# Performance work log

Measured on AMD Instinct MI355X. Metric: run time of the kernel, lower is better.

## Reference

```python
import jax, jax.numpy as jnp
import numpy as np

MAX_SEQ = 2048   # text_max_length: pre-allocated cache length
B = 16           # beam*batch
H = 32           # head_num
D = 128          # head_dim
OFFSET = 2047    # tokens already stored in the cache (decode at last step)
SCALE = float(np.sqrt(D))  # scale_attn = sqrt(head_size), per docstring


def setup_inputs() -> dict:
    key = jax.random.key(0)
    ks = jax.random.split(key, 6)
    query = jax.random.normal(ks[0], (B, 1, H, D), dtype=jnp.float32)
    key_t = jax.random.normal(ks[1], (B, 1, H, D), dtype=jnp.float32)
    value = jax.random.normal(ks[2], (B, 1, H, D), dtype=jnp.float32)
    key_cache = jax.random.normal(ks[3], (MAX_SEQ, B, H, D), dtype=jnp.float32)
    value_cache = jax.random.normal(ks[4], (MAX_SEQ, B, H, D), dtype=jnp.float32)
    # beam_idx[t, b] = parent beam (cache row) of beam b chosen at step t
    beam_idx = jax.random.randint(ks[5], (MAX_SEQ, B), 0, B, dtype=jnp.int32)
    # additive attention mask over [past + current] positions (zeros = no masking;
    # single-token decode query attends to everything causally anyway)
    attention_mask = jnp.zeros((B, 1, 1, OFFSET + 1), dtype=jnp.float32)
    return {
        "query": query, "key": key_t, "value": value,
        "key_cache": key_cache, "value_cache": value_cache,
        "beam_idx": beam_idx, "attention_mask": attention_mask,
        "offset": OFFSET,
    }


def _beam_trace(beam_idx, offset):
    # Back-trace beam ancestry from the latest step to step 0.
    # trace[t, b] = row in the pre-allocated cache that holds token t of the
    # sequence currently occupying beam slot b.
    def step(cur, bi_t):
        new = bi_t[cur]
        return new, new
    init = jnp.arange(B, dtype=beam_idx.dtype)
    _, trace = jax.lax.scan(step, init, beam_idx[:offset], reverse=True)
    return trace  # [offset, B]


def reference(query, key, value, key_cache, value_cache, beam_idx, attention_mask, offset):
    # Indirect gather of KV history via beam-idx indirection.
    trace = _beam_trace(beam_idx, offset)                      # [offset, B]
    idx = trace[:, :, None, None]                              # broadcast over H, D
    k_hist = jnp.take_along_axis(key_cache[:offset], idx, axis=1)   # [offset, B, H, D]
    v_hist = jnp.take_along_axis(value_cache[:offset], idx, axis=1)
    # Append the current token's key/value (equivalent to writing it into the
    # cache at position `offset` and reading it back).
    k_full = jnp.concatenate([k_hist, jnp.transpose(key, (1, 0, 2, 3))], axis=0)    # [offset+1, B, H, D]
    v_full = jnp.concatenate([v_hist, jnp.transpose(value, (1, 0, 2, 3))], axis=0)
    # Scaled dot-product attention (q_len = 1).
    scores = jnp.einsum('bqhd,tbhd->bhqt', query, k_full) / SCALE  # [B, H, 1, offset+1]
    scores = scores + attention_mask
    probs = jax.nn.softmax(scores, axis=-1)
    attn_output = jnp.einsum('bhqt,tbhd->bqhd', probs, v_full)     # [B, 1, H, D]
    return attn_output
```

## Files before the change

kernel.cpp:

```cpp
#include <hip/hip_runtime.h>
#include <math.h>

#define BEAMS 16
#define TMAX  2048
#define HH    32
#define DD    128
#define NSP   24
#define TSM   88
#define KLD   136
#define WLD   40

typedef float          f32x4 __attribute__((ext_vector_type(4)));
typedef short          s16x8 __attribute__((ext_vector_type(8)));
typedef unsigned short u16x8 __attribute__((ext_vector_type(8)));

__device__ __forceinline__ unsigned short f2bf(float f) {
    unsigned x = __float_as_uint(f);
    return (unsigned short)((x + 0x7FFFu + ((x >> 16) & 1u)) >> 16);
}

__device__ __forceinline__ int kofs(int g, int j) {
    return (j < 4) ? (g * 4 + j) : (16 + g * 4 + (j - 4));
}

__global__ __launch_bounds__(1024)
void trace_kernel(const int* __restrict__ beam_idx,
                  const int* __restrict__ offp,
                  int* __restrict__ trace_tb,
                  unsigned long long* __restrict__ slot4_g,
                  int* __restrict__ rowstart_g,
                  int* __restrict__ rows_tu,
                  int* __restrict__ ucnt_g) {
    const int off = *offp;
    const int T   = off + 1;
    const int C   = 8;
    const int NC  = (off + C - 1) / C;

    __shared__ int S[2][256][BEAMS];
    __shared__ unsigned short seen_s[TMAX];

    const int tid = threadIdx.x;
    const int g   = tid >> 4;
    const int j   = tid & 15;
    const int c0 = g, c1 = g + 64, c2 = g + 128, c3 = g + 192;

    {
        int cur0 = j, cur1 = j, cur2 = j, cur3 = j;
        const int hi0 = (c0 < NC) ? min((c0 + 1) * C, off) : 0;
        const int hi1 = (c1 < NC) ? min((c1 + 1) * C, off) : 0;
        const int hi2 = (c2 < NC) ? min((c2 + 1) * C, off) : 0;
        const int hi3 = (c3 < NC) ? min((c3 + 1) * C, off) : 0;
        const int lo0 = c0 * C, lo1 = c1 * C, lo2 = c2 * C, lo3 = c3 * C;
        for (int i = 0; i < C; ++i) {
            const int ta = hi0 - 1 - i;
            if (c0 < NC && ta >= lo0) cur0 = beam_idx[ta * BEAMS + cur0];
            const int tb = hi1 - 1 - i;
            if (c1 < NC && tb >= lo1) cur1 = beam_idx[tb * BEAMS + cur1];
            const int tc = hi2 - 1 - i;
            if (c2 < NC && tc >= lo2) cur2 = beam_idx[tc * BEAMS + cur2];
            const int td = hi3 - 1 - i;
            if (c3 < NC && td >= lo3) cur3 = beam_idx[td * BEAMS + cur3];
        }
        if (c0 < NC) S[0][c0][j] = cur0;
        if (c1 < NC) S[0][c1][j] = cur1;
        if (c2 < NC) S[0][c2][j] = cur2;
        if (c3 < NC) S[0][c3][j] = cur3;
    }
    __syncthreads();

    int rb = 0;
    for (int step = 1; step < NC; step <<= 1) {
        const int wb = rb ^ 1;
        for (int c = g; c < NC; c += 64) {
            int v;
            if (c + step < NC) v = S[rb][c][ S[rb][c + step][j] ];
            else               v = S[rb][c][j];
            S[wb][c][j] = v;
        }
        __syncthreads();
        rb = wb;
    }

    {
        int cur0 = (c0 + 1 < NC) ? S[rb][c0 + 1][j] : j;
        int cur1 = (c1 + 1 < NC) ? S[rb][c1 + 1][j] : j;
        int cur2 = (c2 + 1 < NC) ? S[rb][c2 + 1][j] : j;
        int cur3 = (c3 + 1 < NC) ? S[rb][c3 + 1][j] : j;
        const int hi0 = (c0 < NC) ? min((c0 + 1) * C, off) : 0;
        const int hi1 = (c1 < NC) ? min((c1 + 1) * C, off) : 0;
        const int hi2 = (c2 < NC) ? min((c2 + 1) * C, off) : 0;
        const int hi3 = (c3 < NC) ? min((c3 + 1) * C, off) : 0;
        const int lo0 = c0 * C, lo1 = c1 * C, lo2 = c2 * C, lo3 = c3 * C;
        for (int i = 0; i < C; ++i) {
            const int ta = hi0 - 1 - i;
            if (c0 < NC && ta >= lo0) {
                cur0 = beam_idx[ta * BEAMS + cur0];
                trace_tb[ta * BEAMS + j] = cur0;
            }
            const int tb = hi1 - 1 - i;
            if (c1 < NC && tb >= lo1) {
                cur1 = beam_idx[tb * BEAMS + cur1];
                trace_tb[tb * BEAMS + j] = cur1;
            }
            const int tc = hi2 - 1 - i;
            if (c2 < NC && tc >= lo2) {
                cur2 = beam_idx[tc * BEAMS + cur2];
                trace_tb[tc * BEAMS + j] = cur2;
            }
            const int td = hi3 - 1 - i;
            if (c3 < NC && td >= lo3) {
                cur3 = beam_idx[td * BEAMS + cur3];
                trace_tb[td * BEAMS + j] = cur3;
            }
        }
    }
    __syncthreads();

    for (int t = tid; t < T; t += 1024) {
        if (t == off) {
            seen_s[t]  = 0xFFFFu;
            slot4_g[t] = 0xFEDCBA9876543210ull;
        } else {
            unsigned seen = 0;
            int us[16];
            #pragma unroll
            for (int b2 = 0; b2 < 16; ++b2) {
                us[b2] = trace_tb[t * BEAMS + b2];
                seen |= 1u << us[b2];
            }
            unsigned long long s4 = 0;
            #pragma unroll
            for (int b2 = 0; b2 < 16; ++b2) {
                const unsigned long long sl =
                    (unsigned long long)__popc(seen & ((1u << us[b2]) - 1u));
                s4 |= sl << (4 * b2);
            }
            seen_s[t]  = (unsigned short)seen;
            slot4_g[t] = s4;
        }
    }
    __syncthreads();

    {
        const int wid  = tid >> 6;
        const int lane = tid & 63;
        const int TS   = (T + NSP - 1) / NSP;
        for (int s = wid; s < NSP; s += 16) {
            const int ts0 = s * TS;
            const int ts1 = min(ts0 + TS, T);
            int cum = 0;
            for (int tc0 = ts0; tc0 < ts1; tc0 += 64) {
                const int t = tc0 + lane;
                const bool valid = (t < ts1);
                const unsigned seen = valid ? (unsigned)seen_s[t] : 0u;
                int x = __popc(seen);
                const int n = x;
                #pragma unroll
                for (int o = 1; o < 64; o <<= 1) {
                    const int y = __shfl_up(x, o, 64);
                    if (lane >= o) x += y;
                }
                const int base = cum + x - n;
                if (valid) {
                    rowstart_g[t] = base;
                    int k = 0;
                    for (unsigned m = seen; m; m &= m - 1) {
                        rows_tu[s * 2048 + base + k] = t * 32 + (__ffs(m) - 1);
                        ++k;
                    }
                }
                cum += __shfl(x, 63, 64);
            }
            if (lane == 0) ucnt_g[s] = cum;
        }
    }
}

__device__ __forceinline__ void pv_step(int pb, int w, int n16, int g4,
                                        const unsigned short (&Wt)[2][16][WLD],
                                        const unsigned short (&Vb)[2][32][KLD],
                                        f32x4 (&accO)[4]) {
    union { unsigned long long qw[2]; s16x8 v; } uw;
    uw.qw[0] = *(const unsigned long long*)(&Wt[pb][n16][g4 * 4]);
    uw.qw[1] = *(const unsigned long long*)(&Wt[pb][n16][16 + g4 * 4]);
    #pragma unroll
    for (int dt = 0; dt < 4; ++dt) {
        const int d = ((w - 2) * 4 + dt) * 16 + n16;
        s16x8 bf;
        #pragma unroll
        for (int jj = 0; jj < 8; ++jj)
            bf[jj] = (short)Vb[pb][kofs(g4, jj)][d];
        accO[dt] = __builtin_amdgcn_mfma_f32_16x16x32_bf16(uw.v, bf, accO[dt], 0, 0, 0);
    }
}

__global__ __launch_bounds__(256, 3)
void attn_split_kernel(const float* __restrict__ q,
                       const float* __restrict__ knew,
                       const float* __restrict__ vnew,
                       const float* __restrict__ kc,
                       const float* __restrict__ vc,
                       const float* __restrict__ mask,
                       const unsigned long long* __restrict__ slot4_g,
                       const int* __restrict__ rowstart_g,
                       const int* __restrict__ rows_tu,
                       const int* __restrict__ ucnt_g,
                       const int* __restrict__ offp,
                       float* __restrict__ pl,
                       float* __restrict__ po) {
    const int off = *offp;
    const int T   = off + 1;
    const int TS  = (T + NSP - 1) / NSP;
    const int h   = blockIdx.x / NSP;
    const int s   = blockIdx.x - h * NSP;
    const int ts0 = s * TS;
    const int ts1 = min(ts0 + TS, T);
    const int nts = ts1 - ts0;
    const int U   = ucnt_g[s];
    const int G   = (U + 31) >> 5;

    __shared__ unsigned short Kb[2][32][KLD];
    __shared__ unsigned short Vb[2][32][KLD];
    __shared__ unsigned short Wt[2][16][WLD];
    __shared__ float mask_s[16][TSM];
    __shared__ unsigned long long slot4_s[TSM];
    __shared__ int   rbase_s[TSM];
    __shared__ float ls[2][16];

    const int tid = threadIdx.x;
    const int w   = tid >> 6;
    const int l   = tid & 63;
    const int n16 = l & 15;
    const int g4  = l >> 4;

    for (int i = tid; i < 16 * TSM; i += 256) {
        const int bb = i / TSM, tt = i - bb * TSM;
        mask_s[bb][tt] = (tt < nts) ? mask[(size_t)bb * T + ts0 + tt] : 0.f;
    }
    for (int i = tid; i < nts; i += 256) {
        slot4_s[i] = slot4_g[ts0 + i];
        rbase_s[i] = rowstart_g[ts0 + i];
    }

    const float inv_scale = 0.08838834764831843f;
    s16x8 qf[4];
    {
        const float* qp = q + ((size_t)(n16 * HH + h)) * DD;
        #pragma unroll
        for (int c = 0; c < 4; ++c) {
            const int base = 32 * c + g4 * 4;
            const float4 lo = *(const float4*)(qp + base);
            const float4 hi = *(const float4*)(qp + base + 16);
            qf[c][0] = (short)f2bf(lo.x * inv_scale);
            qf[c][1] = (short)f2bf(lo.y * inv_scale);
            qf[c][2] = (short)f2bf(lo.z * inv_scale);
            qf[c][3] = (short)f2bf(lo.w * inv_scale);
            qf[c][4] = (short)f2bf(hi.x * inv_scale);
            qf[c][5] = (short)f2bf(hi.y * inv_scale);
            qf[c][6] = (short)f2bf(hi.z * inv_scale);
            qf[c][7] = (short)f2bf(hi.w * inv_scale);
        }
    }

    const int r1 = tid >> 4;
    const int cc = tid & 15;
    float4 sk1a, sk1b, sv1a, sv1b, sk2a, sk2b, sv2a, sv2b;

#define LOADR(UU, KA, KB, VA, VB)                                            \
    {                                                                        \
        const int uu = (UU);                                                 \
        const int tu = (uu < U) ? rows_tu[s * 2048 + uu] : 0;                \
        const int t_ = tu >> 5, u_ = tu & 31;                                \
        const float *ks, *vs;                                                \
        if (t_ < off) {                                                      \
            const size_t ro = ((size_t)(t_ * BEAMS + u_) * HH + h) * DD;     \
            ks = kc + ro; vs = vc + ro;                                      \
        } else {                                                             \
            const size_t ro = ((size_t)u_ * HH + h) * DD;                    \
            ks = knew + ro; vs = vnew + ro;                                  \
        }                                                                    \
        KA = *(const float4*)(ks + cc * 8);                                  \
        KB = *(const float4*)(ks + cc * 8 + 4);                              \
        VA = *(const float4*)(vs + cc * 8);                                  \
        VB = *(const float4*)(vs + cc * 8 + 4);                              \
    }

#define PACK8(DST, A, B)                                                     \
    {                                                                        \
        u16x8 p_;                                                            \
        p_[0] = f2bf(A.x); p_[1] = f2bf(A.y); p_[2] = f2bf(A.z);             \
        p_[3] = f2bf(A.w); p_[4] = f2bf(B.x); p_[5] = f2bf(B.y);             \
        p_[6] = f2bf(B.z); p_[7] = f2bf(B.w);                                \
        *(u16x8*)(DST) = p_;                                                 \
    }

    f32x4 accO[4];
    #pragma unroll
    for (int dt = 0; dt < 4; ++dt) accO[dt] = (f32x4){0.f, 0.f, 0.f, 0.f};
    float l_acc = 0.f;

    __syncthreads();

    if (G > 0) { LOADR(0 * 32 + r1, sk1a, sk1b, sv1a, sv1b)
                 LOADR(0 * 32 + r1 + 16, sk2a, sk2b, sv2a, sv2b) }

    for (int g = 0; g < G; ++g) {
        const int buf = g & 1;
        PACK8(&Kb[buf][r1][cc * 8],      sk1a, sk1b)
        PACK8(&Vb[buf][r1][cc * 8],      sv1a, sv1b)
        PACK8(&Kb[buf][r1 + 16][cc * 8], sk2a, sk2b)
        PACK8(&Vb[buf][r1 + 16][cc * 8], sv2a, sv2b)
        if (g + 1 < G) {
            LOADR((g + 1) * 32 + r1, sk1a, sk1b, sv1a, sv1b)
            LOADR((g + 1) * 32 + r1 + 16, sk2a, sk2b, sv2a, sv2b)
        }
        __syncthreads();

        if (w < 2) {
            f32x4 acc = {0.f, 0.f, 0.f, 0.f};
            const unsigned short* krow = &Kb[buf][w * 16 + n16][0];
            #pragma unroll
            for (int c = 0; c < 4; ++c) {
                const unsigned short* ka = krow + 32 * c + g4 * 4;
                union { unsigned long long qw[2]; s16x8 v; } ua;
                ua.qw[0] = *(const unsigned long long*)(ka);
                ua.qw[1] = *(const unsigned long long*)(ka + 16);
                acc = __builtin_amdgcn_mfma_f32_16x16x32_bf16(ua.v, qf[c], acc, 0, 0, 0);
            }
            unsigned short wout[4];
            #pragma unroll
            for (int r = 0; r < 4; ++r) {
                const int u_loc = g * 32 + w * 16 + g4 * 4 + r;
                const bool valid = (u_loc < U);
                const int tu = valid ? rows_tu[s * 2048 + u_loc] : 0;
                const int t_ = tu >> 5;
                int tt = t_ - ts0;
                tt = (tt < 0) ? 0 : tt;
                const unsigned long long s4 = slot4_s[tt];
                const int myslot = (int)((s4 >> (4 * n16)) & 15);
                const int expsl  = u_loc - rbase_s[tt];
                const bool match = valid && (myslot == expsl);
                const float sc = acc[r] + mask_s[n16][tt];
                const float wv = match ? __expf(sc) : 0.f;
                l_acc += wv;
                wout[r] = f2bf(wv);
            }
            const int wc = w * 16 + g4 * 4;
            *(unsigned*)&Wt[buf][n16][wc]     = (unsigned)wout[0] | ((unsigned)wout[1] << 16);
            *(unsigned*)&Wt[buf][n16][wc + 2] = (unsigned)wout[2] | ((unsigned)wout[3] << 16);
        } else if (g > 0) {
            pv_step(buf ^ 1, w, n16, g4, Wt, Vb, accO);
        }
        __syncthreads();
    }
    if (G > 0 && w >= 2) {
        pv_step((G - 1) & 1, w, n16, g4, Wt, Vb, accO);
    }
#undef LOADR
#undef PACK8

    if (w < 2) {
        l_acc += __shfl_xor(l_acc, 16, 64);
        l_acc += __shfl_xor(l_acc, 32, 64);
        if (l < 16) ls[w][n16] = l_acc;
    }
    __syncthreads();
    if (tid < 16)
        pl[((size_t)tid * HH + h) * NSP + s] = ls[0][tid] + ls[1][tid];

    if (w >= 2) {
        #pragma unroll
        for (int dt = 0; dt < 4; ++dt) {
            const int d = ((w - 2) * 4 + dt) * 16 + n16;
            #pragma unroll
            for (int r = 0; r < 4; ++r) {
                const int b = g4 * 4 + r;
                po[((size_t)(b * HH + h) * NSP + s) * DD + d] = accO[dt][r];
            }
        }
    }
}

__global__ __launch_bounds__(128)
void attn_reduce_kernel(const float* __restrict__ pl,
                        const float* __restrict__ po,
                        float* __restrict__ out) {
    const int bh = blockIdx.x;
    const int d  = threadIdx.x;
    float l = 0.f, o = 0.f;
    #pragma unroll 8
    for (int s = 0; s < NSP; ++s) {
        l += pl[(size_t)bh * NSP + s];
        o += po[((size_t)bh * NSP + s) * DD + d];
    }
    out[(size_t)bh * DD + d] = o / l;
}

extern "C" void kernel_launch(void* const* d_in, const int* in_sizes, int n_in,
                              void* d_out, int out_size, void* d_ws, size_t ws_size,
                              hipStream_t stream) {
    const float* q    = (const float*)d_in[0];
    const float* knew = (const float*)d_in[1];
    const float* vnew = (const float*)d_in[2];
    const float* kc   = (const float*)d_in[3];
    const float* vc   = (const float*)d_in[4];
    const int*   bidx = (const int*)d_in[5];
    const float* mask = (const float*)d_in[6];
    const int*   offp = (const int*)d_in[7];

    char* ws = (char*)d_ws;
    int*                trace_tb = (int*)(ws);
    unsigned long long* slot4    = (unsigned long long*)(ws + 131072);
    int*                rowstart = (int*)(ws + 147456);
    int*                rows_tu  = (int*)(ws + 155648);
    int*                ucnt_g   = (int*)(ws + 352256);
    float*              pl       = (float*)(ws + 352768);
    float*              po       = (float*)(ws + 401920);

    hipLaunchKernelGGL(trace_kernel, dim3(1), dim3(1024), 0, stream,
                       bidx, offp, trace_tb, slot4, rowstart, rows_tu,
                       ucnt_g);
    hipLaunchKernelGGL(attn_split_kernel, dim3(HH * NSP), dim3(256), 0, stream,
                       q, knew, vnew, kc, vc, mask,
                       slot4, rowstart, rows_tu, ucnt_g, offp,
                       pl, po);
    hipLaunchKernelGGL(attn_reduce_kernel, dim3(BEAMS * HH), dim3(128), 0, stream,
                       pl, po, (float*)d_out);
}
```

Baseline: 53.54 us.

## Balance split-K partitions by unique cache-row count instead of equal token spans

```diff
diff --git a/kernel.cpp b/kernel.cpp
--- a/kernel.cpp
+++ b/kernel.cpp
@@ -6,7 +6,7 @@
 #define HH    32
 #define DD    128
 #define NSP   24
-#define TSM   88
+#define TSM   128
 #define KLD   136
 #define WLD   40
 
@@ -30,6 +30,7 @@
                   unsigned long long* __restrict__ slot4_g,
                   int* __restrict__ rowstart_g,
                   int* __restrict__ rows_tu,
+                  int* __restrict__ ts_g,
                   int* __restrict__ ucnt_g) {
     const int off = *offp;
     const int T   = off + 1;
@@ -38,6 +39,7 @@
 
     __shared__ int S[2][256][BEAMS];
     __shared__ unsigned short seen_s[TMAX];
+    __shared__ int ts_s[NSP + 1];
 
     const int tid = threadIdx.x;
     const int g   = tid >> 4;
@@ -141,13 +143,58 @@
     }
     __syncthreads();
 
+    int* scanA = &S[0][0][0];
+    int* scanB = &S[1][0][0];
+    for (int t = tid; t < TMAX; t += 1024)
+        scanA[t] = (t < T) ? __popc((unsigned)seen_s[t]) : 0;
+    __syncthreads();
+    int* src = scanA; int* dst = scanB;
+    for (int step = 1; step < TMAX; step <<= 1) {
+        for (int i = tid; i < TMAX; i += 1024)
+            dst[i] = src[i] + ((i >= step) ? src[i - step] : 0);
+        __syncthreads();
+        int* tmp = src; src = dst; dst = tmp;
+    }
+
+    if (tid < 64) {
+        const int total = src[T - 1];
+        const int rps   = (total + NSP - 1) / NSP;
+        const int s     = tid;
+        int fwd;
+        if (s == 0)        fwd = 0;
+        else if (s >= NSP) fwd = T;
+        else {
+            const int target = s * rps;
+            int lo = 0, hi = T;
+            while (lo < hi) {
+                const int mid = (lo + hi) >> 1;
+                const int ex  = (mid > 0) ? src[mid - 1] : 0;
+                if (ex >= target) hi = mid; else lo = mid + 1;
+            }
+            fwd = lo;
+        }
+        int a = (s <= NSP) ? (fwd - s * TSM) : 0x3FFFFFFF;
+        #pragma unroll
+        for (int o = 1; o < 64; o <<= 1) {
+            const int other = __shfl_up(a, o, 64);
+            if (tid >= o) a = min(a, other);
+        }
+        if (s <= NSP) {
+            int ts = s * TSM + a;
+            ts = max(ts, T - (NSP - s) * TSM);
+            ts = max(ts, 0);
+            ts = min(ts, T);
+            ts_s[s] = ts;
+        }
+    }
+    __syncthreads();
+
     {
         const int wid  = tid >> 6;
         const int lane = tid & 63;
-        const int TS   = (T + NSP - 1) / NSP;
         for (int s = wid; s < NSP; s += 16) {
-            const int ts0 = s * TS;
-            const int ts1 = min(ts0 + TS, T);
+            const int ts0 = ts_s[s];
+            const int ts1 = ts_s[s + 1];
             int cum = 0;
             for (int tc0 = ts0; tc0 < ts1; tc0 += 64) {
                 const int t = tc0 + lane;
@@ -174,6 +221,7 @@
             if (lane == 0) ucnt_g[s] = cum;
         }
     }
+    if (tid <= NSP) ts_g[tid] = ts_s[tid];
 }
 
 __device__ __forceinline__ void pv_step(int pb, int w, int n16, int g4,
@@ -204,17 +252,17 @@
                        const unsigned long long* __restrict__ slot4_g,
                        const int* __restrict__ rowstart_g,
                        const int* __restrict__ rows_tu,
+                       const int* __restrict__ ts_g,
                        const int* __restrict__ ucnt_g,
                        const int* __restrict__ offp,
                        float* __restrict__ pl,
                        float* __restrict__ po) {
     const int off = *offp;
     const int T   = off + 1;
-    const int TS  = (T + NSP - 1) / NSP;
     const int h   = blockIdx.x / NSP;
     const int s   = blockIdx.x - h * NSP;
-    const int ts0 = s * TS;
-    const int ts1 = min(ts0 + TS, T);
+    const int ts0 = ts_g[s];
+    const int ts1 = ts_g[s + 1];
     const int nts = ts1 - ts0;
     const int U   = ucnt_g[s];
     const int G   = (U + 31) >> 5;
@@ -234,7 +282,7 @@
     const int g4  = l >> 4;
 
     for (int i = tid; i < 16 * TSM; i += 256) {
-        const int bb = i / TSM, tt = i - bb * TSM;
+        const int bb = i >> 7, tt = i & (TSM - 1);
         mask_s[bb][tt] = (tt < nts) ? mask[(size_t)bb * T + ts0 + tt] : 0.f;
     }
     for (int i = tid; i < nts; i += 256) {
@@ -413,16 +461,17 @@
     unsigned long long* slot4    = (unsigned long long*)(ws + 131072);
     int*                rowstart = (int*)(ws + 147456);
     int*                rows_tu  = (int*)(ws + 155648);
-    int*                ucnt_g   = (int*)(ws + 352256);
-    float*              pl       = (float*)(ws + 352768);
-    float*              po       = (float*)(ws + 401920);
+    int*                ts_g     = (int*)(ws + 352256);
+    int*                ucnt_g   = (int*)(ws + 352768);
+    float*              pl       = (float*)(ws + 353280);
+    float*              po       = (float*)(ws + 402432);
 
     hipLaunchKernelGGL(trace_kernel, dim3(1), dim3(1024), 0, stream,
                        bidx, offp, trace_tb, slot4, rowstart, rows_tu,
-                       ucnt_g);
+                       ts_g, ucnt_g);
     hipLaunchKernelGGL(attn_split_kernel, dim3(HH * NSP), dim3(256), 0, stream,
                        q, knew, vnew, kc, vc, mask,
-                       slot4, rowstart, rows_tu, ucnt_g, offp,
+                       slot4, rowstart, rows_tu, ts_g, ucnt_g, offp,
                        pl, po);
     hipLaunchKernelGGL(attn_reduce_kernel, dim3(BEAMS * HH), dim3(128), 0, stream,
                        pl, po, (float*)d_out);
```

After: 54.79 us. +2.3%, slower.

## Stage beam_idx in LDS as bytes and compute slot masks via wave shuffles

Applied to the files above, without the earlier changes.

```diff
diff --git a/kernel.cpp b/kernel.cpp
--- a/kernel.cpp
+++ b/kernel.cpp
@@ -26,7 +26,6 @@
 __global__ __launch_bounds__(1024)
 void trace_kernel(const int* __restrict__ beam_idx,
                   const int* __restrict__ offp,
-                  int* __restrict__ trace_tb,
                   unsigned long long* __restrict__ slot4_g,
                   int* __restrict__ rowstart_g,
                   int* __restrict__ rows_tu,
@@ -36,13 +35,27 @@
     const int C   = 8;
     const int NC  = (off + C - 1) / C;
 
-    __shared__ int S[2][256][BEAMS];
+    __shared__ unsigned char  bidx_u8[TMAX * BEAMS];
+    __shared__ unsigned char  S[2][256][BEAMS];
     __shared__ unsigned short seen_s[TMAX];
 
     const int tid = threadIdx.x;
     const int g   = tid >> 4;
     const int j   = tid & 15;
     const int c0 = g, c1 = g + 64, c2 = g + 128, c3 = g + 192;
+
+    {
+        const int4* src4 = (const int4*)beam_idx;
+        unsigned*   dst4 = (unsigned*)bidx_u8;
+        #pragma unroll
+        for (int k = 0; k < (TMAX * BEAMS / 4) / 1024; ++k) {
+            const int i4 = k * 1024 + tid;
+            const int4 v = src4[i4];
+            dst4[i4] = (unsigned)(v.x & 15) | ((unsigned)(v.y & 15) << 8)
+                     | ((unsigned)(v.z & 15) << 16) | ((unsigned)(v.w & 15) << 24);
+        }
+    }
+    __syncthreads();
 
     {
         int cur0 = j, cur1 = j, cur2 = j, cur3 = j;
@@ -53,18 +66,18 @@
         const int lo0 = c0 * C, lo1 = c1 * C, lo2 = c2 * C, lo3 = c3 * C;
         for (int i = 0; i < C; ++i) {
             const int ta = hi0 - 1 - i;
-            if (c0 < NC && ta >= lo0) cur0 = beam_idx[ta * BEAMS + cur0];
+            if (c0 < NC && ta >= lo0) cur0 = bidx_u8[ta * BEAMS + cur0];
             const int tb = hi1 - 1 - i;
-            if (c1 < NC && tb >= lo1) cur1 = beam_idx[tb * BEAMS + cur1];
+            if (c1 < NC && tb >= lo1) cur1 = bidx_u8[tb * BEAMS + cur1];
             const int tc = hi2 - 1 - i;
-            if (c2 < NC && tc >= lo2) cur2 = beam_idx[tc * BEAMS + cur2];
+            if (c2 < NC && tc >= lo2) cur2 = bidx_u8[tc * BEAMS + cur2];
             const int td = hi3 - 1 - i;
-            if (c3 < NC && td >= lo3) cur3 = beam_idx[td * BEAMS + cur3];
-        }
-        if (c0 < NC) S[0][c0][j] = cur0;
-        if (c1 < NC) S[0][c1][j] = cur1;
-        if (c2 < NC) S[0][c2][j] = cur2;
-        if (c3 < NC) S[0][c3][j] = cur3;
+            if (c3 < NC && td >= lo3) cur3 = bidx_u8[td * BEAMS + cur3];
+        }
+        if (c0 < NC) S[0][c0][j] = (unsigned char)cur0;
+        if (c1 < NC) S[0][c1][j] = (unsigned char)cur1;
+        if (c2 < NC) S[0][c2][j] = (unsigned char)cur2;
+        if (c3 < NC) S[0][c3][j] = (unsigned char)cur3;
     }
     __syncthreads();
 
@@ -72,7 +85,7 @@
     for (int step = 1; step < NC; step <<= 1) {
         const int wb = rb ^ 1;
         for (int c = g; c < NC; c += 64) {
-            int v;
+            unsigned char v;
             if (c + step < NC) v = S[rb][c][ S[rb][c + step][j] ];
             else               v = S[rb][c][j];
             S[wb][c][j] = v;
@@ -93,51 +106,49 @@
         const int lo0 = c0 * C, lo1 = c1 * C, lo2 = c2 * C, lo3 = c3 * C;
         for (int i = 0; i < C; ++i) {
             const int ta = hi0 - 1 - i;
-            if (c0 < NC && ta >= lo0) {
-                cur0 = beam_idx[ta * BEAMS + cur0];
-                trace_tb[ta * BEAMS + j] = cur0;
-            }
             const int tb = hi1 - 1 - i;
-            if (c1 < NC && tb >= lo1) {
-                cur1 = beam_idx[tb * BEAMS + cur1];
-                trace_tb[tb * BEAMS + j] = cur1;
-            }
             const int tc = hi2 - 1 - i;
-            if (c2 < NC && tc >= lo2) {
-                cur2 = beam_idx[tc * BEAMS + cur2];
-                trace_tb[tc * BEAMS + j] = cur2;
-            }
             const int td = hi3 - 1 - i;
-            if (c3 < NC && td >= lo3) {
-                cur3 = beam_idx[td * BEAMS + cur3];
-                trace_tb[td * BEAMS + j] = cur3;
-            }
-        }
-    }
-    __syncthreads();
-
-    for (int t = tid; t < T; t += 1024) {
-        if (t == off) {
-            seen_s[t]  = 0xFFFFu;
-            slot4_g[t] = 0xFEDCBA9876543210ull;
-        } else {
-            unsigned seen = 0;
-            int us[16];
+            const bool va = (c0 < NC) && (ta >= lo0);
+            const bool vb = (c1 < NC) && (tb >= lo1);
+            const bool vc2 = (c2 < NC) && (tc >= lo2);
+            const bool vd = (c3 < NC) && (td >= lo3);
+            if (va)  cur0 = bidx_u8[ta * BEAMS + cur0];
+            if (vb)  cur1 = bidx_u8[tb * BEAMS + cur1];
+            if (vc2) cur2 = bidx_u8[tc * BEAMS + cur2];
+            if (vd)  cur3 = bidx_u8[td * BEAMS + cur3];
+
+            unsigned m0 = 1u << cur0, m1 = 1u << cur1;
+            unsigned m2 = 1u << cur2, m3 = 1u << cur3;
             #pragma unroll
-            for (int b2 = 0; b2 < 16; ++b2) {
-                us[b2] = trace_tb[t * BEAMS + b2];
-                seen |= 1u << us[b2];
-            }
-            unsigned long long s4 = 0;
+            for (int o = 1; o < 16; o <<= 1) {
+                m0 |= __shfl_xor(m0, o, 64);
+                m1 |= __shfl_xor(m1, o, 64);
+                m2 |= __shfl_xor(m2, o, 64);
+                m3 |= __shfl_xor(m3, o, 64);
+            }
+            unsigned long long s0 = (unsigned long long)__popc(m0 & ((1u << cur0) - 1u)) << (4 * j);
+            unsigned long long s1 = (unsigned long long)__popc(m1 & ((1u << cur1) - 1u)) << (4 * j);
+            unsigned long long s2 = (unsigned long long)__popc(m2 & ((1u << cur2) - 1u)) << (4 * j);
+            unsigned long long s3 = (unsigned long long)__popc(m3 & ((1u << cur3) - 1u)) << (4 * j);
             #pragma unroll
-            for (int b2 = 0; b2 < 16; ++b2) {
-                const unsigned long long sl =
-                    (unsigned long long)__popc(seen & ((1u << us[b2]) - 1u));
-                s4 |= sl << (4 * b2);
-            }
-            seen_s[t]  = (unsigned short)seen;
-            slot4_g[t] = s4;
-        }
+            for (int o = 1; o < 16; o <<= 1) {
+                s0 |= __shfl_xor(s0, o, 64);
+                s1 |= __shfl_xor(s1, o, 64);
+                s2 |= __shfl_xor(s2, o, 64);
+                s3 |= __shfl_xor(s3, o, 64);
+            }
+            if (j == 0) {
+                if (va)  { seen_s[ta] = (unsigned short)m0; slot4_g[ta] = s0; }
+                if (vb)  { seen_s[tb] = (unsigned short)m1; slot4_g[tb] = s1; }
+                if (vc2) { seen_s[tc] = (unsigned short)m2; slot4_g[tc] = s2; }
+                if (vd)  { seen_s[td] = (unsigned short)m3; slot4_g[td] = s3; }
+            }
+        }
+    }
+    if (tid == 0) {
+        seen_s[off]  = 0xFFFFu;
+        slot4_g[off] = 0xFEDCBA9876543210ull;
     }
     __syncthreads();
 
@@ -409,17 +420,15 @@
     const int*   offp = (const int*)d_in[7];
 
     char* ws = (char*)d_ws;
-    int*                trace_tb = (int*)(ws);
-    unsigned long long* slot4    = (unsigned long long*)(ws + 131072);
-    int*                rowstart = (int*)(ws + 147456);
-    int*                rows_tu  = (int*)(ws + 155648);
-    int*                ucnt_g   = (int*)(ws + 352256);
-    float*              pl       = (float*)(ws + 352768);
-    float*              po       = (float*)(ws + 401920);
+    unsigned long long* slot4    = (unsigned long long*)(ws);
+    int*                rowstart = (int*)(ws + 16384);
+    int*                rows_tu  = (int*)(ws + 24576);
+    int*                ucnt_g   = (int*)(ws + 221184);
+    float*              pl       = (float*)(ws + 221696);
+    float*              po       = (float*)(ws + 270848);
 
     hipLaunchKernelGGL(trace_kernel, dim3(1), dim3(1024), 0, stream,
-                       bidx, offp, trace_tb, slot4, rowstart, rows_tu,
-                       ucnt_g);
+                       bidx, offp, slot4, rowstart, rows_tu, ucnt_g);
     hipLaunchKernelGGL(attn_split_kernel, dim3(HH * NSP), dim3(256), 0, stream,
                        q, knew, vnew, kc, vc, mask,
                        slot4, rowstart, rows_tu, ucnt_g, offp,
```

Measured after the change: 60.55 us. +13.1%, slower.
